# Optimization experiments

Measured on AMD Instinct MI355X. Metric: run time of the kernel, lower is better.

Reference implementation:

```python
import jax, jax.numpy as jnp
import numpy as np

DIM = 512
HEADS = 8
DIM_HEAD = DIM // 8          # 64
INNER = HEADS * DIM_HEAD     # 512
M_LANDMARKS = DIM // 2       # 256
PINV_ITERS = 6
RES_KERNEL = 33
LN_EPS = 1e-5


def setup_inputs() -> dict:
    key = jax.random.key(0)
    ks = jax.random.split(key, 7)
    b, n = 8, 4096
    x = jax.random.normal(ks[0], (b, n, DIM), dtype=jnp.float32)
    gamma = jnp.ones((DIM,), jnp.float32)
    beta = jnp.zeros((DIM,), jnp.float32)
    w_qkv = jax.random.normal(ks[1], (DIM, 3 * INNER), jnp.float32) * 0.02
    w_out = jax.random.normal(ks[2], (INNER, DIM), jnp.float32) * 0.02
    b_out = jnp.zeros((DIM,), jnp.float32)
    # depthwise Conv2d(heads, heads, (33,1), groups=heads): torch weight [H,1,33,1]
    res_kernel = jax.random.normal(ks[3], (HEADS, 1, RES_KERNEL, 1), jnp.float32) * 0.05
    return {"x": x, "gamma": gamma, "beta": beta, "w_qkv": w_qkv,
            "w_out": w_out, "b_out": b_out, "res_kernel": res_kernel}


def _moore_penrose_pinv(a, iters=PINV_ITERS):
    # a: [b, h, m, m]
    abs_a = jnp.abs(a)
    col = abs_a.sum(axis=-1).max()   # global max, as in torch.max(col)
    row = abs_a.sum(axis=-2).max()
    z = jnp.swapaxes(a, -1, -2) / (col * row)
    I = jnp.eye(a.shape[-1], dtype=a.dtype)
    for _ in range(iters):
        az = a @ z
        z = 0.25 * z @ (13. * I - az @ (15. * I - az @ (7. * I - az)))
    return z


def _nystrom_attention(xn, w_qkv, res_kernel, w_out, b_out):
    b, n, _ = xn.shape
    h, dh, m = HEADS, DIM_HEAD, M_LANDMARKS
    scale = dh ** -0.5
    qkv = xn @ w_qkv                               # [b, n, 3*inner]
    q, k, v = jnp.split(qkv, 3, axis=-1)
    def to_heads(t):
        return t.reshape(b, n, h, dh).transpose(0, 2, 1, 3)  # [b,h,n,dh]
    q, k, v = to_heads(q), to_heads(k), to_heads(v)
    q = q * scale

    l = n // m  # n chosen as multiple of m -> no padding branch
    # landmark pooling: '(m l) d -> m d' mean
    q_l = q.reshape(b, h, m, l, dh).mean(axis=3)   # [b,h,m,dh]
    k_l = k.reshape(b, h, m, l, dh).mean(axis=3)

    sim1 = jnp.einsum('bhid,bhjd->bhij', q, k_l)    # [b,h,n,m]
    sim2 = jnp.einsum('bhid,bhjd->bhij', q_l, k_l)  # [b,h,m,m]
    sim3 = jnp.einsum('bhid,bhjd->bhij', q_l, k)    # [b,h,m,n]

    attn1 = jax.nn.softmax(sim1, axis=-1)
    attn2 = jax.nn.softmax(sim2, axis=-1)
    attn3 = jax.nn.softmax(sim3, axis=-1)

    attn2_inv = _moore_penrose_pinv(attn2)
    out = (attn1 @ attn2_inv) @ (attn3 @ v)         # [b,h,n,dh]

    # residual depthwise conv over sequence dim (kernel 33x1, groups=heads)
    pad = RES_KERNEL // 2
    out = out + jax.lax.conv_general_dilated(
        v, res_kernel, window_strides=(1, 1),
        padding=((pad, pad), (0, 0)),
        dimension_numbers=('NCHW', 'OIHW', 'NCHW'),
        feature_group_count=HEADS)

    out = out.transpose(0, 2, 1, 3).reshape(b, n, h * dh)  # [b,n,inner]
    return out @ w_out + b_out  # dropout omitted (eval mode)


def reference(x, gamma, beta, w_qkv, w_out, b_out, res_kernel):
    mu = x.mean(axis=-1, keepdims=True)
    var = x.var(axis=-1, keepdims=True)
    xn = (x - mu) * jax.lax.rsqrt(var + LN_EPS) * gamma + beta
    return x + _nystrom_attention(xn, w_qkv, res_kernel, w_out, b_out)
```

## Files before the change

kernel.cpp:

```cpp
#include <hip/hip_runtime.h>

#define SEQ 4096
#define DMODEL 512
#define NH 8
#define DH 64
#define MLM 256
#define NBH 64
#define NROWS 32768

typedef unsigned short bf16_t;
typedef __attribute__((ext_vector_type(8))) short bf16x8;
typedef __attribute__((ext_vector_type(4))) float f32x4;

__device__ __forceinline__ float bf2f(unsigned short u) {
  return __uint_as_float(((unsigned)u) << 16);
}
__device__ __forceinline__ unsigned short f2bf(float f) {
  unsigned u = __float_as_uint(f);
  u += 0x7fffu + ((u >> 16) & 1u);
  return (unsigned short)(u >> 16);
}
__device__ __forceinline__ void unp8(const bf16_t* p, float* d) {
  uint4 u = *(const uint4*)p;
  d[0] = __uint_as_float(u.x << 16); d[1] = __uint_as_float(u.x & 0xffff0000u);
  d[2] = __uint_as_float(u.y << 16); d[3] = __uint_as_float(u.y & 0xffff0000u);
  d[4] = __uint_as_float(u.z << 16); d[5] = __uint_as_float(u.z & 0xffff0000u);
  d[6] = __uint_as_float(u.w << 16); d[7] = __uint_as_float(u.w & 0xffff0000u);
}

__device__ __forceinline__ void gll(const void* g, void* l) {
  __builtin_amdgcn_global_load_lds(
      (const __attribute__((address_space(1))) unsigned int*)g,
      (__attribute__((address_space(3))) unsigned int*)l, 16, 0, 0);
}

__global__ __launch_bounds__(64) void ln_kernel(const float* __restrict__ x,
    const float* __restrict__ gamma, const float* __restrict__ beta,
    bf16_t* __restrict__ xn) {
  int row = blockIdx.x;
  const float4* xr = (const float4*)(x + (size_t)row * DMODEL);
  int t = threadIdx.x;
  float4 a = xr[t], b = xr[t + 64];
  float s  = a.x + a.y + a.z + a.w + b.x + b.y + b.z + b.w;
  float ss = a.x*a.x + a.y*a.y + a.z*a.z + a.w*a.w
           + b.x*b.x + b.y*b.y + b.z*b.z + b.w*b.w;
#pragma unroll
  for (int off = 32; off > 0; off >>= 1) {
    s  += __shfl_xor(s, off);
    ss += __shfl_xor(ss, off);
  }
  float mean = s * (1.0f / DMODEL);
  float var  = ss * (1.0f / DMODEL) - mean * mean;
  float rstd = rsqrtf(var + 1e-5f);
  const float4* g4 = (const float4*)gamma;
  const float4* be4 = (const float4*)beta;
  ushort4* o = (ushort4*)(xn + (size_t)row * DMODEL);
  float4 g = g4[t], bb = be4[t];
  ushort4 r;
  r.x = f2bf((a.x - mean) * rstd * g.x + bb.x);
  r.y = f2bf((a.y - mean) * rstd * g.y + bb.y);
  r.z = f2bf((a.z - mean) * rstd * g.z + bb.z);
  r.w = f2bf((a.w - mean) * rstd * g.w + bb.w);
  o[t] = r;
  g = g4[t + 64]; bb = be4[t + 64];
  r.x = f2bf((b.x - mean) * rstd * g.x + bb.x);
  r.y = f2bf((b.y - mean) * rstd * g.y + bb.y);
  r.z = f2bf((b.z - mean) * rstd * g.z + bb.z);
  r.w = f2bf((b.w - mean) * rstd * g.w + bb.w);
  o[t + 64] = r;
}

__global__ __launch_bounds__(256) void convT(const float* __restrict__ w,
    bf16_t* __restrict__ wt, int K, int N) {
  size_t idx = (size_t)blockIdx.x * 256 + threadIdx.x;
  int n = (int)(idx / K), k = (int)(idx % K);
  wt[idx] = f2bf(w[(size_t)k * N + n]);
}

#define MFMA_GEMM_BODY(APTR, BTPTR, KDIM) \
  __shared__ short As[128][32]; \
  __shared__ short Bs[128][32]; \
  int tid = threadIdx.x; \
  int lane = tid & 63; \
  int wv = tid >> 6; \
  int wm = (wv & 1) << 6, wn = (wv >> 1) << 6; \
  int l15 = lane & 15, l16 = lane >> 4; \
  f32x4 acc[4][4]; \
  _Pragma("unroll") for (int fm = 0; fm < 4; ++fm) \
    _Pragma("unroll") for (int fn = 0; fn < 4; ++fn) \
      acc[fm][fn] = (f32x4){0.f, 0.f, 0.f, 0.f}; \
  int ar0 = tid >> 2, ac0 = (tid & 3) << 3; \
  const bf16_t* Ab  = (APTR) + (size_t)(m0 + ar0) * (KDIM) + ac0; \
  const bf16_t* Ab1 = (APTR) + (size_t)(m0 + ar0 + 64) * (KDIM) + ac0; \
  const bf16_t* Bb  = (BTPTR) + (size_t)(n0 + ar0) * (KDIM) + ac0; \
  const bf16_t* Bb1 = (BTPTR) + (size_t)(n0 + ar0 + 64) * (KDIM) + ac0; \
  short* AsW  = &As[(wv << 4)][0]; \
  short* AsW1 = &As[64 + (wv << 4)][0]; \
  short* BsW  = &Bs[(wv << 4)][0]; \
  short* BsW1 = &Bs[64 + (wv << 4)][0]; \
  for (int k0 = 0; k0 < (KDIM); k0 += 32) { \
    gll(Ab + k0, AsW);  gll(Ab1 + k0, AsW1); \
    gll(Bb + k0, BsW);  gll(Bb1 + k0, BsW1); \
    __syncthreads(); \
    bf16x8 af[4], bfr[4]; \
    _Pragma("unroll") for (int f = 0; f < 4; ++f) { \
      af[f]  = *(const bf16x8*)&As[wm + f * 16 + l15][l16 * 8]; \
      bfr[f] = *(const bf16x8*)&Bs[wn + f * 16 + l15][l16 * 8]; \
    } \
    _Pragma("unroll") for (int fm = 0; fm < 4; ++fm) \
      _Pragma("unroll") for (int fn = 0; fn < 4; ++fn) \
        acc[fm][fn] = __builtin_amdgcn_mfma_f32_16x16x32_bf16(af[fm], bfr[fn], acc[fm][fn], 0, 0, 0); \
    __syncthreads(); \
  }

__global__ __launch_bounds__(512) void gemm_qkv_256(const bf16_t* __restrict__ A,
    const bf16_t* __restrict__ BT, bf16_t* __restrict__ q, bf16_t* __restrict__ k,
    bf16_t* __restrict__ v, bf16_t* __restrict__ vT) {
  int bid = blockIdx.x;
  int orig = (bid & 7) * 96 + (bid >> 3);
  int n0 = (orig % 6) << 8;
  int m0 = (orig / 6) << 8;
  __shared__ short As[4][8192];
  __shared__ short Bs[4][8192];
  int tid = threadIdx.x;
  int lane = tid & 63;
  int wid = tid >> 6;
  int wr = wid >> 2, wc = wid & 3;
  int l15 = lane & 15, l16 = lane >> 4;
  int sl = (l16 ^ (l15 & 3)) << 3;
  int gr  = lane >> 2;
  int gcs = ((lane & 3) ^ ((lane >> 2) & 3)) << 3;
  f32x4 acc[8][4];
#pragma unroll
  for (int fm = 0; fm < 8; ++fm)
#pragma unroll
    for (int fn = 0; fn < 4; ++fn) acc[fm][fn] = (f32x4){0.f, 0.f, 0.f, 0.f};

#define STAGE(kt, s) { \
    _Pragma("unroll") for (int u = 0; u < 2; ++u) { \
      int r0 = (wid << 5) + (u << 4); \
      gll(A  + (size_t)(m0 + r0 + gr) * 512 + (kt) * 32 + gcs, &As[s][r0 << 5]); \
      gll(BT + (size_t)(n0 + r0 + gr) * 512 + (kt) * 32 + gcs, &Bs[s][r0 << 5]); \
    } }

  STAGE(0, 0) STAGE(1, 1) STAGE(2, 2)
  for (int t = 0; t < 16; ++t) {
    int s = t & 3;
    if (t < 14)       asm volatile("s_waitcnt vmcnt(8)" ::: "memory");
    else if (t == 14) asm volatile("s_waitcnt vmcnt(4)" ::: "memory");
    else              asm volatile("s_waitcnt vmcnt(0)" ::: "memory");
    __builtin_amdgcn_s_barrier();
    if (t + 3 < 16) STAGE(t + 3, ((t + 3) & 3))
    bf16x8 a[8], b[4];
#pragma unroll
    for (int fm = 0; fm < 8; ++fm)
      a[fm] = *(const bf16x8*)&As[s][(((wr << 7) + (fm << 4) + l15) << 5) + sl];
#pragma unroll
    for (int fn = 0; fn < 4; ++fn)
      b[fn] = *(const bf16x8*)&Bs[s][(((wc << 6) + (fn << 4) + l15) << 5) + sl];
    asm volatile("s_waitcnt lgkmcnt(0)" ::: "memory");
    __builtin_amdgcn_sched_barrier(0);
    __builtin_amdgcn_s_setprio(1);
#pragma unroll
    for (int fm = 0; fm < 8; ++fm)
#pragma unroll
      for (int fn = 0; fn < 4; ++fn)
        acc[fm][fn] = __builtin_amdgcn_mfma_f32_16x16x32_bf16(a[fm], b[fn], acc[fm][fn], 0, 0, 0);
    __builtin_amdgcn_s_setprio(0);
  }
#undef STAGE
#pragma unroll
  for (int fm = 0; fm < 8; ++fm) {
    int row0 = m0 + (wr << 7) + (fm << 4) + (l16 << 2);
    int bat = row0 >> 12;
    int nn0 = row0 & 4095;
#pragma unroll
    for (int fn = 0; fn < 4; ++fn) {
      int col = n0 + (wc << 6) + (fn << 4) + l15;
      int which = col >> 9;
      int hd = (col >> 6) & 7;
      int d  = col & 63;
      if (which == 2) {
        ushort4 pk;
        pk.x = f2bf(acc[fm][fn][0]); pk.y = f2bf(acc[fm][fn][1]);
        pk.z = f2bf(acc[fm][fn][2]); pk.w = f2bf(acc[fm][fn][3]);
        *(ushort4*)(vT + ((size_t)(bat * NH + hd) * DH + d) * SEQ + nn0) = pk;
#pragma unroll
        for (int rg = 0; rg < 4; ++rg)
          v[(((size_t)(bat * NH + hd)) * SEQ + nn0 + rg) * DH + d] = f2bf(acc[fm][fn][rg]);
      } else {
        bf16_t* dst = (which == 0) ? q : k;
        float scale = (which == 0) ? 0.125f : 1.f;
#pragma unroll
        for (int rg = 0; rg < 4; ++rg)
          dst[(((size_t)(bat * NH + hd)) * SEQ + nn0 + rg) * DH + d] = f2bf(acc[fm][fn][rg] * scale);
      }
    }
  }
}

__global__ __launch_bounds__(256) void gemm_out_mfma(const bf16_t* __restrict__ A,
    const bf16_t* __restrict__ BT, const float* __restrict__ bias,
    const float* __restrict__ x, float* __restrict__ y) {
  int bid = blockIdx.x;
  int orig = (bid & 7) * 128 + (bid >> 3);
  int n0 = (orig & 3) << 7;
  int m0 = (orig >> 2) << 7;
  MFMA_GEMM_BODY(A, BT, 512)
#pragma unroll
  for (int fm = 0; fm < 4; ++fm) {
#pragma unroll
    for (int fn = 0; fn < 4; ++fn) {
      int col = n0 + wn + fn * 16 + l15;
      float bv = bias[col];
#pragma unroll
      for (int rg = 0; rg < 4; ++rg) {
        int row = m0 + wm + fm * 16 + l16 * 4 + rg;
        y[(size_t)row * DMODEL + col] = x[(size_t)row * DMODEL + col] + acc[fm][fn][rg] + bv;
      }
    }
  }
}

__global__ __launch_bounds__(256) void bmm_mfma32(const bf16_t* __restrict__ Ag,
    const bf16_t* __restrict__ BTg, bf16_t* __restrict__ Cb,
    bf16_t* __restrict__ CTb, float* __restrict__ Cf,
    int K, float alpha, float eA, float diagc, int flags) {
  int bid = blockIdx.x;
  int orig = (bid & 7) * 512 + (bid >> 3);
  int bh = orig >> 6;
  int tile = orig & 63;
  int n0 = (tile & 7) << 5;
  int m0 = (tile >> 3) << 5;
  const bf16_t* A  = Ag + (size_t)bh * 256 * K;
  const bf16_t* BT = BTg + (size_t)bh * 256 * K;
  __shared__ short As[32][36];
  __shared__ short Bs[32][36];
  int tid = threadIdx.x;
  int lane = tid & 63;
  int wv = tid >> 6;
  int wm = (wv & 1) << 4, wn = (wv >> 1) << 4;
  int l15 = lane & 15, l16 = lane >> 4;
  f32x4 acc = (f32x4){0.f, 0.f, 0.f, 0.f};
  int ar0 = tid >> 3, ac0 = (tid & 7) << 2;
  const bf16_t* Ab = A + (size_t)(m0 + ar0) * K + ac0;
  const bf16_t* Bb = BT + (size_t)(n0 + ar0) * K + ac0;
  uint2 ga = *(const uint2*)Ab;
  uint2 gb = *(const uint2*)Bb;
  for (int k0 = 0; k0 < K; k0 += 32) {
    *(uint2*)&As[ar0][ac0] = ga;
    *(uint2*)&Bs[ar0][ac0] = gb;
    __syncthreads();
    if (k0 + 32 < K) {
      ga = *(const uint2*)(Ab + k0 + 32);
      gb = *(const uint2*)(Bb + k0 + 32);
    }
    bf16x8 af = *(const bf16x8*)&As[wm + l15][l16 * 8];
    bf16x8 bf = *(const bf16x8*)&Bs[wn + l15][l16 * 8];
    acc = __builtin_amdgcn_mfma_f32_16x16x32_bf16(af, bf, acc, 0, 0, 0);
    __syncthreads();
  }
  size_t cbase = (size_t)bh * 65536;
  int row0 = m0 + wm + l16 * 4;
  int col = n0 + wn + l15;
  float v4[4];
#pragma unroll
  for (int rg = 0; rg < 4; ++rg) {
    float val = alpha * acc[rg];
    if (eA != 0.f) val += eA * bf2f(A[(size_t)(row0 + rg) * K + col]);
    if (row0 + rg == col) val += diagc;
    v4[rg] = val;
  }
  if (flags & 1) {
#pragma unroll
    for (int rg = 0; rg < 4; ++rg)
      Cb[cbase + (size_t)(row0 + rg) * 256 + col] = f2bf(v4[rg]);
  }
  if (flags & 2) {
    ushort4 pk;
    pk.x = f2bf(v4[0]); pk.y = f2bf(v4[1]);
    pk.z = f2bf(v4[2]); pk.w = f2bf(v4[3]);
    *(ushort4*)(CTb + cbase + (size_t)col * 256 + row0) = pk;
  }
  if (flags & 4) {
#pragma unroll
    for (int rg = 0; rg < 4; ++rg)
      Cf[cbase + (size_t)(row0 + rg) * 256 + col] = v4[rg];
  }
}

__global__ __launch_bounds__(256) void ns_zy32(const bf16_t* __restrict__ zg,
    const bf16_t* __restrict__ Yg, const bf16_t* __restrict__ t1Tg,
    bf16_t* __restrict__ zog, bf16_t* __restrict__ Yog,
    bf16_t* __restrict__ YTog) {
  int bid = blockIdx.x;
  int orig = (bid & 7) * 1024 + (bid >> 3);
  int task = orig >> 6;
  int bh = task >> 1;
  int which = task & 1;
  int tile = orig & 63;
  int n0 = (tile & 7) << 5;
  int m0 = (tile >> 3) << 5;
  const bf16_t* A  = (which ? Yg : zg) + ((size_t)bh << 16);
  const bf16_t* BT = t1Tg + ((size_t)bh << 16);
  __shared__ short As[32][36];
  __shared__ short Bs[32][36];
  int tid = threadIdx.x;
  int lane = tid & 63;
  int wv = tid >> 6;
  int wm = (wv & 1) << 4, wn = (wv >> 1) << 4;
  int l15 = lane & 15, l16 = lane >> 4;
  f32x4 acc = (f32x4){0.f, 0.f, 0.f, 0.f};
  int ar0 = tid >> 3, ac0 = (tid & 7) << 2;
  const bf16_t* Ab = A + (size_t)(m0 + ar0) * 256 + ac0;
  const bf16_t* Bb = BT + (size_t)(n0 + ar0) * 256 + ac0;
  uint2 ga = *(const uint2*)Ab;
  uint2 gb = *(const uint2*)Bb;
  for (int k0 = 0; k0 < 256; k0 += 32) {
    *(uint2*)&As[ar0][ac0] = ga;
    *(uint2*)&Bs[ar0][ac0] = gb;
    __syncthreads();
    if (k0 + 32 < 256) {
      ga = *(const uint2*)(Ab + k0 + 32);
      gb = *(const uint2*)(Bb + k0 + 32);
    }
    bf16x8 af = *(const bf16x8*)&As[wm + l15][l16 * 8];
    bf16x8 bf = *(const bf16x8*)&Bs[wn + l15][l16 * 8];
    acc = __builtin_amdgcn_mfma_f32_16x16x32_bf16(af, bf, acc, 0, 0, 0);
    __syncthreads();
  }
  size_t cbase = (size_t)bh << 16;
  int row0 = m0 + wm + l16 * 4;
  int col = n0 + wn + l15;
  float v4[4];
#pragma unroll
  for (int rg = 0; rg < 4; ++rg) v4[rg] = 0.25f * acc[rg];
  if (which == 0) {
#pragma unroll
    for (int rg = 0; rg < 4; ++rg)
      zog[cbase + (size_t)(row0 + rg) * 256 + col] = f2bf(v4[rg]);
  } else {
#pragma unroll
    for (int rg = 0; rg < 4; ++rg)
      Yog[cbase + (size_t)(row0 + rg) * 256 + col] = f2bf(v4[rg]);
    ushort4 pk;
    pk.x = f2bf(v4[0]); pk.y = f2bf(v4[1]);
    pk.z = f2bf(v4[2]); pk.w = f2bf(v4[3]);
    *(ushort4*)(YTog + cbase + (size_t)col * 256 + row0) = pk;
  }
}

__global__ __launch_bounds__(64) void pool_kernel(const bf16_t* __restrict__ q,
    const bf16_t* __restrict__ k, bf16_t* __restrict__ qlb,
    bf16_t* __restrict__ klb) {
  int bh = blockIdx.y, i = blockIdx.x, d = threadIdx.x;
  const bf16_t* qb = q + ((size_t)bh * SEQ + i * 16) * DH + d;
  const bf16_t* kb = k + ((size_t)bh * SEQ + i * 16) * DH + d;
  float sq = 0.f, sk = 0.f;
#pragma unroll
  for (int j = 0; j < 16; ++j) { sq += bf2f(qb[j * DH]); sk += bf2f(kb[j * DH]); }
  sq *= (1.f / 16.f); sk *= (1.f / 16.f);
  qlb[((size_t)bh * MLM + i) * DH + d] = f2bf(sq);
  klb[((size_t)bh * MLM + i) * DH + d] = f2bf(sk);
}

__global__ __launch_bounds__(256) void softmax256(const float* __restrict__ af,
    bf16_t* __restrict__ ab) {
  const float* ar = af + (size_t)blockIdx.x * MLM;
  int t = threadIdx.x;
  float v = ar[t];
  __shared__ float redm[4], reds[4];
  float m = v;
#pragma unroll
  for (int off = 32; off > 0; off >>= 1) m = fmaxf(m, __shfl_xor(m, off));
  if ((t & 63) == 0) redm[t >> 6] = m;
  __syncthreads();
  m = fmaxf(fmaxf(redm[0], redm[1]), fmaxf(redm[2], redm[3]));
  float p = __expf(v - m);
  float s = p;
#pragma unroll
  for (int off = 32; off > 0; off >>= 1) s += __shfl_xor(s, off);
  if ((t & 63) == 0) reds[t >> 6] = s;
  __syncthreads();
  s = reds[0] + reds[1] + reds[2] + reds[3];
  ab[(size_t)blockIdx.x * MLM + t] = f2bf(p / s);
}

__global__ void init_scal(unsigned* s) { if (threadIdx.x < 2) s[threadIdx.x] = 0u; }

__global__ __launch_bounds__(256) void colrow_max(const bf16_t* __restrict__ a,
    unsigned* __restrict__ scal) {
  int bh = blockIdx.x;
  int task = blockIdx.y;
  const bf16_t* ab = a + (size_t)bh * MLM * MLM;
  int t = threadIdx.x;
  float s = 0.f;
  if (task == 0) {
    const bf16_t* rp = ab + (size_t)t * MLM;
    for (int j = 0; j < MLM; j += 8) {
      float d[8];
      unp8(rp + j, d);
      s += d[0]; s += d[1]; s += d[2]; s += d[3];
      s += d[4]; s += d[5]; s += d[6]; s += d[7];
    }
  } else {
    for (int i = 0; i < MLM; ++i) s += bf2f(ab[(size_t)i * MLM + t]);
  }
  __shared__ float red[4];
  float m = s;
#pragma unroll
  for (int off = 32; off > 0; off >>= 1) m = fmaxf(m, __shfl_xor(m, off));
  if ((t & 63) == 0) red[t >> 6] = m;
  __syncthreads();
  if (t == 0) {
    m = fmaxf(fmaxf(red[0], red[1]), fmaxf(red[2], red[3]));
    atomicMax(scal + task, __float_as_uint(m));
  }
}

__global__ __launch_bounds__(256) void zinit(const bf16_t* __restrict__ ab,
    bf16_t* __restrict__ z0, bf16_t* __restrict__ z0T,
    const unsigned* __restrict__ scal) {
  size_t idx = (size_t)blockIdx.x * 256 + threadIdx.x;
  float denom = __uint_as_float(scal[0]) * __uint_as_float(scal[1]);
  size_t bh = idx >> 16;
  int i = (int)((idx >> 8) & 255);
  int j = (int)(idx & 255);
  bf16_t r = f2bf(bf2f(ab[idx]) / denom);
  z0T[idx] = r;
  z0[(bh << 16) + ((size_t)j << 8) + i] = r;
}

__global__ __launch_bounds__(64) void attn3v_mfma(const bf16_t* __restrict__ qlb,
    const bf16_t* __restrict__ kg, const bf16_t* __restrict__ vT,
    float* __restrict__ pacc, float* __restrict__ pm, float* __restrict__ ps) {
  int bid = blockIdx.x;
  int orig = (bid & 7) * 512 + (bid >> 3);
  int m0 = (orig & 7) << 5;
  int cz = (orig >> 3) & 7;
  int bh = orig >> 6;
  int lane = threadIdx.x;
  int l15 = lane & 15, l16 = lane >> 4;
  __shared__ short plds[32][136];
  const bf16_t* qbase = qlb + (size_t)bh * MLM * DH;
  const bf16_t* kbase = kg + (size_t)bh * SEQ * DH;
  const bf16_t* vbase = vT + (size_t)bh * DH * SEQ;
  bf16x8 af[2][2];
#pragma unroll
  for (int mt = 0; mt < 2; ++mt)
#pragma unroll
    for (int ks = 0; ks < 2; ++ks)
      af[mt][ks] = *(const bf16x8*)(qbase + (size_t)(m0 + mt * 16 + l15) * DH + ks * 32 + l16 * 8);
  float m_run[2][4], s_run[2][4];
  f32x4 o[2][4];
#pragma unroll
  for (int mt = 0; mt < 2; ++mt) {
#pragma unroll
    for (int rg = 0; rg < 4; ++rg) { m_run[mt][rg] = -1e30f; s_run[mt][rg] = 0.f; }
#pragma unroll
    for (int n2 = 0; n2 < 4; ++n2) o[mt][n2] = (f32x4){0.f, 0.f, 0.f, 0.f};
  }
  int kbeg = cz << 9;
  for (int kt = kbeg; kt < kbeg + 512; kt += 128) {
    f32x4 sacc[2][8];
#pragma unroll
    for (int mt = 0; mt < 2; ++mt)
#pragma unroll
      for (int nt = 0; nt < 8; ++nt) sacc[mt][nt] = (f32x4){0.f, 0.f, 0.f, 0.f};
#pragma unroll
    for (int nt = 0; nt < 8; ++nt) {
      const bf16_t* kr = kbase + (size_t)(kt + nt * 16 + l15) * DH + l16 * 8;
      bf16x8 b0 = *(const bf16x8*)kr;
      bf16x8 b1 = *(const bf16x8*)(kr + 32);
      sacc[0][nt] = __builtin_amdgcn_mfma_f32_16x16x32_bf16(af[0][0], b0, sacc[0][nt], 0, 0, 0);
      sacc[0][nt] = __builtin_amdgcn_mfma_f32_16x16x32_bf16(af[0][1], b1, sacc[0][nt], 0, 0, 0);
      sacc[1][nt] = __builtin_amdgcn_mfma_f32_16x16x32_bf16(af[1][0], b0, sacc[1][nt], 0, 0, 0);
      sacc[1][nt] = __builtin_amdgcn_mfma_f32_16x16x32_bf16(af[1][1], b1, sacc[1][nt], 0, 0, 0);
    }
#pragma unroll
    for (int mt = 0; mt < 2; ++mt)
#pragma unroll
      for (int rg = 0; rg < 4; ++rg) {
        float mx = sacc[mt][0][rg];
#pragma unroll
        for (int nt = 1; nt < 8; ++nt) mx = fmaxf(mx, sacc[mt][nt][rg]);
        mx = fmaxf(mx, __shfl_xor(mx, 1));
        mx = fmaxf(mx, __shfl_xor(mx, 2));
        mx = fmaxf(mx, __shfl_xor(mx, 4));
        mx = fmaxf(mx, __shfl_xor(mx, 8));
        float mnew = fmaxf(m_run[mt][rg], mx);
        float corr = __expf(m_run[mt][rg] - mnew);
        float s = 0.f;
#pragma unroll
        for (int nt = 0; nt < 8; ++nt) {
          float p = __expf(sacc[mt][nt][rg] - mnew);
          sacc[mt][nt][rg] = p;
          s += p;
        }
        s += __shfl_xor(s, 1); s += __shfl_xor(s, 2);
        s += __shfl_xor(s, 4); s += __shfl_xor(s, 8);
        s_run[mt][rg] = s_run[mt][rg] * corr + s;
        m_run[mt][rg] = mnew;
#pragma unroll
        for (int n2 = 0; n2 < 4; ++n2) o[mt][n2][rg] *= corr;
      }
#pragma unroll
    for (int mt = 0; mt < 2; ++mt)
#pragma unroll
      for (int nt = 0; nt < 8; ++nt)
#pragma unroll
        for (int rg = 0; rg < 4; ++rg)
          plds[mt * 16 + l16 * 4 + rg][nt * 16 + l15] = (short)f2bf(sacc[mt][nt][rg]);
#pragma unroll
    for (int ks2 = 0; ks2 < 4; ++ks2) {
      bf16x8 pa0 = *(const bf16x8*)&plds[l15][ks2 * 32 + l16 * 8];
      bf16x8 pa1 = *(const bf16x8*)&plds[16 + l15][ks2 * 32 + l16 * 8];
#pragma unroll
      for (int n2 = 0; n2 < 4; ++n2) {
        bf16x8 vb8 = *(const bf16x8*)(vbase + (size_t)(n2 * 16 + l15) * SEQ + kt + ks2 * 32 + l16 * 8);
        o[0][n2] = __builtin_amdgcn_mfma_f32_16x16x32_bf16(pa0, vb8, o[0][n2], 0, 0, 0);
        o[1][n2] = __builtin_amdgcn_mfma_f32_16x16x32_bf16(pa1, vb8, o[1][n2], 0, 0, 0);
      }
    }
  }
  size_t pidx0 = (size_t)(bh * 8 + cz) * MLM + m0;
#pragma unroll
  for (int mt = 0; mt < 2; ++mt)
#pragma unroll
    for (int n2 = 0; n2 < 4; ++n2)
#pragma unroll
      for (int rg = 0; rg < 4; ++rg) {
        int row = mt * 16 + l16 * 4 + rg;
        pacc[(pidx0 + row) * 64 + n2 * 16 + l15] = o[mt][n2][rg];
      }
  if (l15 == 0) {
#pragma unroll
    for (int mt = 0; mt < 2; ++mt)
#pragma unroll
      for (int rg = 0; rg < 4; ++rg) {
        pm[pidx0 + mt * 16 + l16 * 4 + rg] = m_run[mt][rg];
        ps[pidx0 + mt * 16 + l16 * 4 + rg] = s_run[mt][rg];
      }
  }
}

__global__ __launch_bounds__(256) void attn3v_comb(const float* __restrict__ pacc,
    const float* __restrict__ pm, const float* __restrict__ ps,
    bf16_t* __restrict__ a3vb) {
  int gw = blockIdx.x * 4 + (threadIdx.x >> 6);
  int lane = threadIdx.x & 63;
  int bh = gw >> 8, row = gw & 255;
  float ms[8];
  float M = -1e30f;
#pragma unroll
  for (int cc = 0; cc < 8; ++cc) {
    ms[cc] = pm[(size_t)(bh * 8 + cc) * MLM + row];
    M = fmaxf(M, ms[cc]);
  }
  float S = 0.f, val = 0.f;
#pragma unroll
  for (int cc = 0; cc < 8; ++cc) {
    size_t pidx = (size_t)(bh * 8 + cc) * MLM + row;
    float w = __expf(ms[cc] - M);
    S += w * ps[pidx];
    val += w * pacc[pidx * 64 + lane];
  }
  a3vb[(size_t)gw * 64 + lane] = f2bf(val / S);
}

__global__ __launch_bounds__(256) void wm_kernel(const bf16_t* __restrict__ zb,
    const bf16_t* __restrict__ a3vb, bf16_t* __restrict__ wmT) {
  int bh = blockIdx.y;
  int m0 = blockIdx.x << 6;
  __shared__ bf16_t a3s[MLM * DH];
  int t = threadIdx.x;
  const bf16_t* asrc = a3vb + (size_t)bh * MLM * DH;
#pragma unroll
  for (int i = 0; i < 8; ++i)
    *(bf16x8*)(a3s + ((size_t)t + 256 * i) * 8) =
        *(const bf16x8*)(asrc + ((size_t)t + 256 * i) * 8);
  __syncthreads();
  int row = m0 + (t >> 2);
  int c0 = (t & 3) * 16;
  const bf16_t* zrow = zb + (size_t)bh * 65536 + (size_t)row * 256;
  float acc16[16] = {};
  for (int k0 = 0; k0 < 256; k0 += 8) {
    float a8[8];
    unp8(zrow + k0, a8);
#pragma unroll
    for (int j = 0; j < 8; ++j) {
      float av[16];
      unp8(a3s + (k0 + j) * 64 + c0, av);
      unp8(a3s + (k0 + j) * 64 + c0 + 8, av + 8);
#pragma unroll
      for (int e = 0; e < 16; ++e) acc16[e] += a8[j] * av[e];
    }
  }
  bf16_t* wd = wmT + (size_t)bh * DH * MLM;
#pragma unroll
  for (int e = 0; e < 16; ++e)
    wd[(size_t)(c0 + e) * MLM + row] = f2bf(acc16[e]);
}

__global__ __launch_bounds__(64) void attn1_mfma(const bf16_t* __restrict__ qg,
    const bf16_t* __restrict__ klb, const bf16_t* __restrict__ wmT,
    bf16_t* __restrict__ om) {
  int bh = blockIdx.y, bat = bh >> 3, head = bh & 7;
  int m0 = blockIdx.x << 5;
  int lane = threadIdx.x;
  int l15 = lane & 15, l16 = lane >> 4;
  __shared__ short plds[32][264];
  const bf16_t* qbase = qg + (size_t)bh * SEQ * DH;
  const bf16_t* kbase = klb + (size_t)bh * MLM * DH;
  bf16x8 af[2][2];
#pragma unroll
  for (int mt = 0; mt < 2; ++mt)
#pragma unroll
    for (int ks = 0; ks < 2; ++ks)
      af[mt][ks] = *(const bf16x8*)(qbase + (size_t)(m0 + mt * 16 + l15) * DH + ks * 32 + l16 * 8);
  f32x4 acc[2][16];
#pragma unroll
  for (int mt = 0; mt < 2; ++mt)
#pragma unroll
    for (int nt = 0; nt < 16; ++nt) acc[mt][nt] = (f32x4){0.f, 0.f, 0.f, 0.f};
#pragma unroll
  for (int nt = 0; nt < 16; ++nt) {
    bf16x8 b0 = *(const bf16x8*)(kbase + (size_t)(nt * 16 + l15) * DH + l16 * 8);
    bf16x8 b1 = *(const bf16x8*)(kbase + (size_t)(nt * 16 + l15) * DH + 32 + l16 * 8);
    acc[0][nt] = __builtin_amdgcn_mfma_f32_16x16x32_bf16(af[0][0], b0, acc[0][nt], 0, 0, 0);
    acc[0][nt] = __builtin_amdgcn_mfma_f32_16x16x32_bf16(af[0][1], b1, acc[0][nt], 0, 0, 0);
    acc[1][nt] = __builtin_amdgcn_mfma_f32_16x16x32_bf16(af[1][0], b0, acc[1][nt], 0, 0, 0);
    acc[1][nt] = __builtin_amdgcn_mfma_f32_16x16x32_bf16(af[1][1], b1, acc[1][nt], 0, 0, 0);
  }
  float inv[2][4];
#pragma unroll
  for (int mt = 0; mt < 2; ++mt)
#pragma unroll
    for (int rg = 0; rg < 4; ++rg) {
      float mx = acc[mt][0][rg];
#pragma unroll
      for (int nt = 1; nt < 16; ++nt) mx = fmaxf(mx, acc[mt][nt][rg]);
      mx = fmaxf(mx, __shfl_xor(mx, 1));
      mx = fmaxf(mx, __shfl_xor(mx, 2));
      mx = fmaxf(mx, __shfl_xor(mx, 4));
      mx = fmaxf(mx, __shfl_xor(mx, 8));
      float s = 0.f;
#pragma unroll
      for (int nt = 0; nt < 16; ++nt) {
        float p = __expf(acc[mt][nt][rg] - mx);
        acc[mt][nt][rg] = p;
        s += p;
      }
      s += __shfl_xor(s, 1); s += __shfl_xor(s, 2);
      s += __shfl_xor(s, 4); s += __shfl_xor(s, 8);
      inv[mt][rg] = 1.f / s;
    }
#pragma unroll
  for (int mt = 0; mt < 2; ++mt)
#pragma unroll
    for (int nt = 0; nt < 16; ++nt)
#pragma unroll
      for (int rg = 0; rg < 4; ++rg)
        plds[mt * 16 + l16 * 4 + rg][nt * 16 + l15] = (short)f2bf(acc[mt][nt][rg]);
  const bf16_t* wbase = wmT + (size_t)bh * DH * MLM;
  f32x4 o[2][4];
#pragma unroll
  for (int mt = 0; mt < 2; ++mt)
#pragma unroll
    for (int n2 = 0; n2 < 4; ++n2) o[mt][n2] = (f32x4){0.f, 0.f, 0.f, 0.f};
#pragma unroll
  for (int ks = 0; ks < 8; ++ks) {
    bf16x8 pa0 = *(const bf16x8*)&plds[l15][ks * 32 + l16 * 8];
    bf16x8 pa1 = *(const bf16x8*)&plds[16 + l15][ks * 32 + l16 * 8];
#pragma unroll
    for (int n2 = 0; n2 < 4; ++n2) {
      bf16x8 wb = *(const bf16x8*)(wbase + (size_t)(n2 * 16 + l15) * MLM + ks * 32 + l16 * 8);
      o[0][n2] = __builtin_amdgcn_mfma_f32_16x16x32_bf16(pa0, wb, o[0][n2], 0, 0, 0);
      o[1][n2] = __builtin_amdgcn_mfma_f32_16x16x32_bf16(pa1, wb, o[1][n2], 0, 0, 0);
    }
  }
#pragma unroll
  for (int mt = 0; mt < 2; ++mt)
#pragma unroll
    for (int n2 = 0; n2 < 4; ++n2)
#pragma unroll
      for (int rg = 0; rg < 4; ++rg) {
        int n = m0 + mt * 16 + l16 * 4 + rg;
        int d = n2 * 16 + l15;
        om[((size_t)(bat * SEQ + n)) * DMODEL + head * DH + d] =
            f2bf(o[mt][n2][rg] * inv[mt][rg]);
      }
}

__global__ __launch_bounds__(256) void conv_add(const bf16_t* __restrict__ vg,
    const float* __restrict__ rk, bf16_t* __restrict__ om) {
  int bh = blockIdx.y, bat = bh >> 3, head = bh & 7;
  int n0 = blockIdx.x << 5;
  __shared__ bf16_t vs[64 * 64];
  int t = threadIdx.x;
  const bf16_t* vbase = vg + (size_t)bh * SEQ * DH;
#pragma unroll
  for (int i = 0; i < 2; ++i) {
    int li = t + 256 * i;
    int rr = li >> 3, cc = (li & 7) << 3;
    int src = n0 - 16 + rr;
    bf16x8 val;
    if (src >= 0 && src < SEQ) val = *(const bf16x8*)(vbase + (size_t)src * DH + cc);
    else { short z = 0; val = (bf16x8){z, z, z, z, z, z, z, z}; }
    *(bf16x8*)(vs + rr * 64 + cc) = val;
  }
  __syncthreads();
  float w[33];
#pragma unroll
  for (int i = 0; i < 33; ++i) w[i] = rk[head * 33 + i];
  int d = t & 63;
  int r0 = (t >> 6) << 3;
  float out[8] = {0.f, 0.f, 0.f, 0.f, 0.f, 0.f, 0.f, 0.f};
#pragma unroll
  for (int j = 0; j < 40; ++j) {
    float vv = bf2f(vs[(r0 + j) * 64 + d]);
    int ilo = j - 32; if (ilo < 0) ilo = 0;
    int ihi = j; if (ihi > 7) ihi = 7;
    for (int i = ilo; i <= ihi; ++i) out[i] += w[j - i] * vv;
  }
#pragma unroll
  for (int i = 0; i < 8; ++i) {
    int n = n0 + r0 + i;
    size_t idx = ((size_t)(bat * SEQ + n)) * DMODEL + head * DH + d;
    om[idx] = f2bf(bf2f(om[idx]) + out[i]);
  }
}

extern "C" void kernel_launch(void* const* d_in, const int* in_sizes, int n_in,
                              void* d_out, int out_size, void* d_ws, size_t ws_size,
                              hipStream_t stream) {
  const float* x     = (const float*)d_in[0];
  const float* gamma = (const float*)d_in[1];
  const float* beta  = (const float*)d_in[2];
  const float* w_qkv = (const float*)d_in[3];
  const float* w_out = (const float*)d_in[4];
  const float* b_out = (const float*)d_in[5];
  const float* rk    = (const float*)d_in[6];
  float* y  = (float*)d_out;

  bf16_t* xnb  = (bf16_t*)d_ws;
  bf16_t* qb   = xnb + 16777216;
  bf16_t* kb   = qb + 16777216;
  bf16_t* vb   = kb + 16777216;
  bf16_t* wqkvT = vb + 16777216;
  bf16_t* woutT = wqkvT + 786432;
  bf16_t* qlb  = woutT + 262144;
  bf16_t* klb  = qlb + 1048576;
  bf16_t* a2b  = klb + 1048576;
  bf16_t* zA   = a2b + 4194304;
  bf16_t* z0T  = zA + 4194304;
  bf16_t* zB   = z0T + 4194304;
  bf16_t* Ya   = zB + 4194304;
  bf16_t* Yb   = z0T;
  bf16_t* vTb  = zA;
  bf16_t* a3vb = Ya + 4194304;
  bf16_t* wmT  = a3vb + 1048576;
  float*  SR   = (float*)(wmT + 1048576);
  float*  a2f  = SR;
  float*  pacc = SR;
  bf16_t* YTa  = (bf16_t*)SR;
  bf16_t* YTb  = YTa + 4194304;
  bf16_t* t2T  = YTa + 8388608;
  bf16_t* t1T  = YTa + 12582912;
  float*  pm   = SR + 8388608;
  float*  ps   = pm + 131072;
  unsigned* scal = (unsigned*)(ps + 131072);
  size_t need = (size_t)93323264 * 2 + (size_t)(8388608 + 262144) * 4 + 64;
  if (ws_size < need) return;

  ln_kernel<<<NROWS, 64, 0, stream>>>(x, gamma, beta, xnb);
  convT<<<3072, 256, 0, stream>>>(w_qkv, wqkvT, 512, 1536);
  convT<<<1024, 256, 0, stream>>>(w_out, woutT, 512, 512);

  gemm_qkv_256<<<768, 512, 0, stream>>>(xnb, wqkvT, qb, kb, vb, vTb);
  pool_kernel<<<dim3(MLM, NBH), 64, 0, stream>>>(qb, kb, qlb, klb);

  bmm_mfma32<<<4096, 256, 0, stream>>>(qlb, klb, nullptr, nullptr, a2f,
      64, 1.f, 0.f, 0.f, 4);
  softmax256<<<NBH * MLM, 256, 0, stream>>>(a2f, a2b);

  init_scal<<<1, 64, 0, stream>>>(scal);
  colrow_max<<<dim3(NBH, 2), 256, 0, stream>>>(a2b, scal);

  attn3v_mfma<<<4096, 64, 0, stream>>>(qlb, kb, vTb, pacc, pm, ps);
  attn3v_comb<<<4096, 256, 0, stream>>>(pacc, pm, ps, a3vb);

  zinit<<<16384, 256, 0, stream>>>(a2b, zA, z0T, scal);
  bmm_mfma32<<<4096, 256, 0, stream>>>(a2b, z0T, Ya, YTa, nullptr,
      256, 1.f, 0.f, 0.f, 3);
  bf16_t* zc = zA;  bf16_t* zo = zB;
  bf16_t* Yc = Ya;  bf16_t* YTc = YTa;
  bf16_t* Yo = Yb;  bf16_t* YTo = YTb;
  for (int it = 0; it < 6; ++it) {
    bmm_mfma32<<<4096, 256, 0, stream>>>(Yc, YTc, nullptr, t2T, nullptr,
        256, 1.f, -7.f, 15.f, 2);
    bmm_mfma32<<<4096, 256, 0, stream>>>(Yc, t2T, nullptr, t1T, nullptr,
        256, -1.f, 0.f, 13.f, 2);
    ns_zy32<<<8192, 256, 0, stream>>>(zc, Yc, t1T, zo, Yo, YTo);
    bf16_t* tp;
    tp = zc; zc = zo; zo = tp;
    tp = Yc; Yc = Yo; Yo = tp;
    tp = YTc; YTc = YTo; YTo = tp;
  }

  wm_kernel<<<dim3(4, NBH), 256, 0, stream>>>(zc, a3vb, wmT);

  bf16_t* om = xnb;
  attn1_mfma<<<dim3(SEQ / 32, NBH), 64, 0, stream>>>(qb, klb, wmT, om);
  conv_add<<<dim3(SEQ / 32, NBH), 256, 0, stream>>>(vb, rk, om);

  gemm_out_mfma<<<1024, 256, 0, stream>>>(om, woutT, b_out, x, y);
}
```

Before: 766.9 us.

## Fuse landmark pooling into QKV GEMM epilogue and drop row-major V copy

The QKV GEMM epilogue now computes the 16-row landmark means of q and k with cross-lane shuffles and writes qlb/klb directly, which removes the separate pool kernel and its re-read of q and k. The row-major V output is no longer written. The conv_add kernel instead reads the transposed vT buffer, and vT gets its own workspace slot instead of aliasing zA. This cuts one launch and about 32 MB of scattered stores, at the cost of a strided transposing load into shared memory in conv_add and extra shuffles in the GEMM epilogue.

Result: no change. 758.0 us (-1.2%).

```diff
diff --git a/kernel.cpp b/kernel.cpp
--- a/kernel.cpp
+++ b/kernel.cpp
@@ -115,7 +115,7 @@
 
 __global__ __launch_bounds__(512) void gemm_qkv_256(const bf16_t* __restrict__ A,
     const bf16_t* __restrict__ BT, bf16_t* __restrict__ q, bf16_t* __restrict__ k,
-    bf16_t* __restrict__ v, bf16_t* __restrict__ vT) {
+    bf16_t* __restrict__ vT, bf16_t* __restrict__ qlb, bf16_t* __restrict__ klb) {
   int bid = blockIdx.x;
   int orig = (bid & 7) * 96 + (bid >> 3);
   int n0 = (orig % 6) << 8;
@@ -174,6 +174,7 @@
     int row0 = m0 + (wr << 7) + (fm << 4) + (l16 << 2);
     int bat = row0 >> 12;
     int nn0 = row0 & 4095;
+    int lm  = nn0 >> 4;
 #pragma unroll
     for (int fn = 0; fn < 4; ++fn) {
       int col = n0 + (wc << 6) + (fn << 4) + l15;
@@ -185,15 +186,19 @@
         pk.x = f2bf(acc[fm][fn][0]); pk.y = f2bf(acc[fm][fn][1]);
         pk.z = f2bf(acc[fm][fn][2]); pk.w = f2bf(acc[fm][fn][3]);
         *(ushort4*)(vT + ((size_t)(bat * NH + hd) * DH + d) * SEQ + nn0) = pk;
-#pragma unroll
-        for (int rg = 0; rg < 4; ++rg)
-          v[(((size_t)(bat * NH + hd)) * SEQ + nn0 + rg) * DH + d] = f2bf(acc[fm][fn][rg]);
       } else {
         bf16_t* dst = (which == 0) ? q : k;
         float scale = (which == 0) ? 0.125f : 1.f;
 #pragma unroll
         for (int rg = 0; rg < 4; ++rg)
           dst[(((size_t)(bat * NH + hd)) * SEQ + nn0 + rg) * DH + d] = f2bf(acc[fm][fn][rg] * scale);
+        float s = acc[fm][fn][0] + acc[fm][fn][1] + acc[fm][fn][2] + acc[fm][fn][3];
+        s += __shfl_xor(s, 16);
+        s += __shfl_xor(s, 32);
+        if (l16 == 0) {
+          bf16_t* pdst = (which == 0) ? qlb : klb;
+          pdst[((size_t)(bat * NH + hd) * MLM + lm) * DH + d] = f2bf(s * scale * 0.0625f);
+        }
       }
     }
   }
@@ -350,20 +355,6 @@
   }
 }
 
-__global__ __launch_bounds__(64) void pool_kernel(const bf16_t* __restrict__ q,
-    const bf16_t* __restrict__ k, bf16_t* __restrict__ qlb,
-    bf16_t* __restrict__ klb) {
-  int bh = blockIdx.y, i = blockIdx.x, d = threadIdx.x;
-  const bf16_t* qb = q + ((size_t)bh * SEQ + i * 16) * DH + d;
-  const bf16_t* kb = k + ((size_t)bh * SEQ + i * 16) * DH + d;
-  float sq = 0.f, sk = 0.f;
-#pragma unroll
-  for (int j = 0; j < 16; ++j) { sq += bf2f(qb[j * DH]); sk += bf2f(kb[j * DH]); }
-  sq *= (1.f / 16.f); sk *= (1.f / 16.f);
-  qlb[((size_t)bh * MLM + i) * DH + d] = f2bf(sq);
-  klb[((size_t)bh * MLM + i) * DH + d] = f2bf(sk);
-}
-
 __global__ __launch_bounds__(256) void softmax256(const float* __restrict__ af,
     bf16_t* __restrict__ ab) {
   const float* ar = af + (size_t)blockIdx.x * MLM;
@@ -692,28 +683,37 @@
       }
 }
 
-__global__ __launch_bounds__(256) void conv_add(const bf16_t* __restrict__ vg,
+__global__ __launch_bounds__(256) void conv_add(const bf16_t* __restrict__ vT,
     const float* __restrict__ rk, bf16_t* __restrict__ om) {
   int bh = blockIdx.y, bat = bh >> 3, head = bh & 7;
   int n0 = blockIdx.x << 5;
   __shared__ bf16_t vs[64 * 64];
   int t = threadIdx.x;
-  const bf16_t* vbase = vg + (size_t)bh * SEQ * DH;
-#pragma unroll
-  for (int i = 0; i < 2; ++i) {
-    int li = t + 256 * i;
-    int rr = li >> 3, cc = (li & 7) << 3;
-    int src = n0 - 16 + rr;
-    bf16x8 val;
-    if (src >= 0 && src < SEQ) val = *(const bf16x8*)(vbase + (size_t)src * DH + cc);
-    else { short z = 0; val = (bf16x8){z, z, z, z, z, z, z, z}; }
-    *(bf16x8*)(vs + rr * 64 + cc) = val;
+  int d = t & 63;
+  int nq = (t >> 6) << 4;
+  const bf16_t* vrow = vT + ((size_t)bh * DH + d) * SEQ;
+#pragma unroll
+  for (int h = 0; h < 2; ++h) {
+    int nb = n0 - 16 + nq + h * 8;
+    unsigned short tmp[8];
+    if (nb >= 0 && nb + 8 <= SEQ) {
+      bf16x8 val = *(const bf16x8*)(vrow + nb);
+#pragma unroll
+      for (int e = 0; e < 8; ++e) tmp[e] = ((unsigned short*)&val)[e];
+    } else {
+#pragma unroll
+      for (int e = 0; e < 8; ++e) {
+        int n = nb + e;
+        tmp[e] = (n >= 0 && n < SEQ) ? vrow[n] : (unsigned short)0;
+      }
+    }
+#pragma unroll
+    for (int e = 0; e < 8; ++e) vs[(nq + h * 8 + e) * 64 + d] = tmp[e];
   }
   __syncthreads();
   float w[33];
 #pragma unroll
   for (int i = 0; i < 33; ++i) w[i] = rk[head * 33 + i];
-  int d = t & 63;
   int r0 = (t >> 6) << 3;
   float out[8] = {0.f, 0.f, 0.f, 0.f, 0.f, 0.f, 0.f, 0.f};
 #pragma unroll
@@ -746,8 +746,8 @@
   bf16_t* xnb  = (bf16_t*)d_ws;
   bf16_t* qb   = xnb + 16777216;
   bf16_t* kb   = qb + 16777216;
-  bf16_t* vb   = kb + 16777216;
-  bf16_t* wqkvT = vb + 16777216;
+  bf16_t* vTb  = kb + 16777216;
+  bf16_t* wqkvT = vTb + 16777216;
   bf16_t* woutT = wqkvT + 786432;
   bf16_t* qlb  = woutT + 262144;
   bf16_t* klb  = qlb + 1048576;
@@ -757,7 +757,6 @@
   bf16_t* zB   = z0T + 4194304;
   bf16_t* Ya   = zB + 4194304;
   bf16_t* Yb   = z0T;
-  bf16_t* vTb  = zA;
   bf16_t* a3vb = Ya + 4194304;
   bf16_t* wmT  = a3vb + 1048576;
   float*  SR   = (float*)(wmT + 1048576);
@@ -777,8 +776,7 @@
   convT<<<3072, 256, 0, stream>>>(w_qkv, wqkvT, 512, 1536);
   convT<<<1024, 256, 0, stream>>>(w_out, woutT, 512, 512);
 
-  gemm_qkv_256<<<768, 512, 0, stream>>>(xnb, wqkvT, qb, kb, vb, vTb);
-  pool_kernel<<<dim3(MLM, NBH), 64, 0, stream>>>(qb, kb, qlb, klb);
+  gemm_qkv_256<<<768, 512, 0, stream>>>(xnb, wqkvT, qb, kb, vTb, qlb, klb);
 
   bmm_mfma32<<<4096, 256, 0, stream>>>(qlb, klb, nullptr, nullptr, a2f,
       64, 1.f, 0.f, 0.f, 4);
@@ -812,7 +810,7 @@
 
   bf16_t* om = xnb;
   attn1_mfma<<<dim3(SEQ / 32, NBH), 64, 0, stream>>>(qb, klb, wmT, om);
-  conv_add<<<dim3(SEQ / 32, NBH), 256, 0, stream>>>(vb, rk, om);
+  conv_add<<<dim3(SEQ / 32, NBH), 256, 0, stream>>>(vTb, rk, om);
 
   gemm_out_mfma<<<1024, 256, 0, stream>>>(om, woutT, b_out, x, y);
 }
```
